# Kernel optimization log

Measured on AMD Instinct MI355X. Metric: run time of the kernel, lower is better.

Reference implementation:

```python
import jax, jax.numpy as jnp
import numpy as np

B, S, D = 1, 2048, 2048
H = 16            # num query heads
QL = 1536         # q_lora_rank
KVL = 512         # kv_lora_rank
DN = 128          # qk_nope_head_dim
DR = 64           # qk_rope_head_dim
DV = 128          # v_head_dim
F = 8192          # ffn intermediate
EPS = 1e-6
WAVE = 10000.0


def _rms(x, scale, eps=EPS):
    # fp32 norm then cast back, matching DeepSeekV3_1RMSNorm
    x32 = x.astype(jnp.float32)
    ms = jnp.mean(x32 * x32, axis=-1, keepdims=True)
    return (x32 * jax.lax.rsqrt(ms + eps)).astype(x.dtype) * scale


def _rope_tables(seq_len, dim):
    inv_freq = 1.0 / (WAVE ** (jnp.arange(0, dim, 2, dtype=jnp.float32) / dim))
    t = jnp.arange(seq_len, dtype=jnp.float32)[:, None] * inv_freq[None, :]  # [S, dim/2]
    emb = jnp.concatenate([t, t], axis=-1)  # [S, dim]
    return jnp.cos(emb), jnp.sin(emb)


def _apply_rope(x, cos, sin):
    # x: [B, S, H, dr]; rotate-half convention
    half = x.shape[-1] // 2
    x1, x2 = x[..., :half], x[..., half:]
    rot = jnp.concatenate([-x2, x1], axis=-1)
    return x * cos[None, :, None, :] + rot * sin[None, :, None, :]


def setup_inputs() -> dict:
    key = jax.random.key(0)
    ks = jax.random.split(key, 12)
    w = lambda k, shp: (jax.random.normal(k, shp, dtype=jnp.float32) * 0.02)
    inp = {
        "hidden_states": jax.random.normal(ks[0], (B, S, D), dtype=jnp.float32),
        "attention_mask": jnp.broadcast_to(jnp.tril(jnp.ones((S, S), dtype=bool)), (B, S, S)),
        "pre_attn_scale": jnp.ones((D,), jnp.float32),
        "wqa": w(ks[1], (D, QL)),
        "q_norm_scale": jnp.ones((QL,), jnp.float32),
        "wqb": w(ks[2], (QL, H * (DN + DR))),
        "wkva": w(ks[3], (D, KVL + DR)),
        "kv_norm_scale": jnp.ones((KVL,), jnp.float32),
        "wkvb": w(ks[4], (KVL, H * (DN + DV))),
        "wo": w(ks[5], (H * DV, D)),
        "pre_ffn_scale": jnp.ones((D,), jnp.float32),
        "wg": w(ks[6], (D, F)),
        "bg": jnp.zeros((F,), jnp.float32),
        "wu": w(ks[7], (D, F)),
        "bu": jnp.zeros((F,), jnp.float32),
        "wd": w(ks[8], (F, D)),
        "bd": jnp.zeros((D,), jnp.float32),
    }
    return inp


def reference(hidden_states, attention_mask, pre_attn_scale, wqa, q_norm_scale, wqb,
              wkva, kv_norm_scale, wkvb, wo, pre_ffn_scale, wg, bg, wu, bu, wd, bd):
    x = hidden_states
    # --- pre-attention RMSNorm ---
    n = _rms(x, pre_attn_scale)
    # --- MLA attention ---
    q = (_rms(n @ wqa, q_norm_scale) @ wqb).reshape(B, S, H, DN + DR)
    q_nope, q_rope = q[..., :DN], q[..., DN:]
    kva = n @ wkva                              # [B,S,KVL+DR]
    c_kv, k_rope = kva[..., :KVL], kva[..., KVL:]
    kv = (_rms(c_kv, kv_norm_scale) @ wkvb).reshape(B, S, H, DN + DV)
    k_nope, v = kv[..., :DN], kv[..., DN:]
    cos, sin = _rope_tables(S, DR)
    q_rope = _apply_rope(q_rope, cos, sin)
    k_rope = _apply_rope(k_rope[:, :, None, :], cos, sin)  # [B,S,1,DR] shared across heads
    qf = jnp.concatenate([q_nope, q_rope], axis=-1)
    kf = jnp.concatenate([k_nope, jnp.broadcast_to(k_rope, (B, S, H, DR))], axis=-1)
    scale = 1.0 / float(np.sqrt(DN + DR))
    scores = jnp.einsum('bqhd,bkhd->bhqk', qf, kf) * scale
    scores = jnp.where(attention_mask[:, None, :, :], scores, jnp.float32(-1e9))
    probs = jax.nn.softmax(scores, axis=-1)
    attn = jnp.einsum('bhqk,bkhd->bqhd', probs, v).reshape(B, S, H * DV)
    x = x + attn @ wo                            # residual 1 (dropout=0)
    # --- pre-FFN RMSNorm + dense SwiGLU FFN ---
    n = _rms(x, pre_ffn_scale)
    ff = (jax.nn.silu(n @ wg + bg) * (n @ wu + bu)) @ wd + bd
    return x + ff                                # residual 2
```

## Files before the change

kernel.cpp:

```cpp
#include <hip/hip_runtime.h>
#include <hip/hip_bf16.h>
#include <stdint.h>

typedef unsigned short u16;
using f32x4  = __attribute__((ext_vector_type(4))) float;
using bf16x8 = __attribute__((ext_vector_type(8))) __bf16;
using u32x4  = __attribute__((ext_vector_type(4))) uint32_t;
using u16x4  = __attribute__((ext_vector_type(4))) unsigned short;
using u16x8  = __attribute__((ext_vector_type(8))) unsigned short;

#define S_LEN 2048
#define DM    2048
#define NH    16
#define QLR   1536
#define KVLR  512
#define DNOPE 128
#define DROPE 64
#define DVAL  128
#define FFD   8192

static __device__ __forceinline__ float bf2f(u16 u) {
    union { uint32_t i; float f; } v; v.i = ((uint32_t)u) << 16; return v.f;
}
static __device__ __forceinline__ u16 f2bf(float f) {
    union { float f; uint32_t i; } v; v.f = f;
    uint32_t x = v.i;
    return (u16)((x + 0x7FFF + ((x >> 16) & 1)) >> 16);
}
static __device__ __forceinline__ void gload16(const u16* g, const u16* l) {
    __builtin_amdgcn_global_load_lds(
        (const __attribute__((address_space(1))) void*)g,
        (__attribute__((address_space(3))) void*)l, 16, 0, 0);
}

struct TWJob { const float* src; u16* dst; int R, C, xt, start; };
struct TWJobs { TWJob j[8]; };

__global__ __launch_bounds__(256)
void transpose_all(TWJobs jobs)
{
    __shared__ __align__(16) u16 tile[64][68];
    const int bid = blockIdx.x;
    int e = 0;
#pragma unroll
    for (int i = 1; i < 8; ++i) e = (bid >= jobs.j[i].start) ? i : e;
    const float* src = jobs.j[e].src;
    u16* dst = jobs.j[e].dst;
    const int R = jobs.j[e].R, C = jobs.j[e].C;
    const int local = bid - jobs.j[e].start;
    const int c0 = (local % jobs.j[e].xt) * 64;
    const int r0 = (local / jobs.j[e].xt) * 64;
    const int t = threadIdx.x;
#pragma unroll
    for (int i = 0; i < 4; ++i) {
        int idx = i * 256 + t;
        int r = idx >> 4, c4 = idx & 15;
        float4 v = *reinterpret_cast<const float4*>(&src[(size_t)(r0 + r) * C + c0 + c4 * 4]);
        u16x4 b; b[0] = f2bf(v.x); b[1] = f2bf(v.y); b[2] = f2bf(v.z); b[3] = f2bf(v.w);
        *reinterpret_cast<u16x4*>(&tile[r][c4 * 4]) = b;
    }
    __syncthreads();
#pragma unroll
    for (int i = 0; i < 4; ++i) {
        int idx = i * 256 + t;
        int rr = idx >> 4, k4 = idx & 15;
        u16x4 o;
#pragma unroll
        for (int j = 0; j < 4; ++j) o[j] = tile[k4 * 4 + j][rr];
        *reinterpret_cast<u16x4*>(&dst[(size_t)(c0 + rr) * R + r0 + k4 * 4]) = o;
    }
}

__global__ __launch_bounds__(256)
void transpose_v(const u16* __restrict__ kv, u16* __restrict__ vt)
{
    __shared__ __align__(16) u16 tile[64][76];
    const int t = threadIdx.x;
    const int s0 = blockIdx.x * 64;
    const int d0 = blockIdx.y * 64;
    const int h  = blockIdx.z;
#pragma unroll
    for (int i = 0; i < 2; ++i) {
        int idx = i * 256 + t;
        int s = idx >> 3, c8 = idx & 7;
        u16x8 v = *reinterpret_cast<const u16x8*>(kv + (size_t)(s0 + s) * (NH * 256) + h * 256 + 128 + d0 + c8 * 8);
        u16x4 lo, hi;
#pragma unroll
        for (int j = 0; j < 4; ++j) { lo[j] = v[j]; hi[j] = v[4 + j]; }
        *reinterpret_cast<u16x4*>(&tile[s][c8 * 8])     = lo;
        *reinterpret_cast<u16x4*>(&tile[s][c8 * 8 + 4]) = hi;
    }
    __syncthreads();
#pragma unroll
    for (int i = 0; i < 4; ++i) {
        int idx = i * 256 + t;
        int d = idx >> 4, s4 = idx & 15;
        u16x4 o;
#pragma unroll
        for (int j = 0; j < 4; ++j) o[j] = tile[s4 * 4 + j][d];
        *reinterpret_cast<u16x4*>(&vt[(size_t)(h * 128 + d0 + d) * S_LEN + s0 + s4 * 4]) = o;
    }
}

template<bool IN_F32>
__global__ __launch_bounds__(256)
void rms_norm(const void* __restrict__ in, int in_stride, int width,
              const float* __restrict__ scale, u16* __restrict__ out, int out_stride)
{
    const int row = blockIdx.x;
    const int t = threadIdx.x;
    const float* inf = (const float*)in;
    const u16*   inb = (const u16*)in;
    float ss = 0.f;
    for (int c = t; c < width; c += 256) {
        float v = IN_F32 ? inf[(size_t)row * in_stride + c] : bf2f(inb[(size_t)row * in_stride + c]);
        ss += v * v;
    }
#pragma unroll
    for (int o = 32; o > 0; o >>= 1) ss += __shfl_xor(ss, o);
    __shared__ float red[4];
    if ((t & 63) == 0) red[t >> 6] = ss;
    __syncthreads();
    float inv = rsqrtf((red[0] + red[1] + red[2] + red[3]) / (float)width + 1e-6f);
    for (int c = t; c < width; c += 256) {
        float v = IN_F32 ? inf[(size_t)row * in_stride + c] : bf2f(inb[(size_t)row * in_stride + c]);
        out[(size_t)row * out_stride + c] = f2bf(v * inv * scale[c]);
    }
}

__global__ __launch_bounds__(256)
void rope_qk(u16* __restrict__ q, const float* __restrict__ kva, u16* __restrict__ kr)
{
    const int s = blockIdx.x;
    const int t = threadIdx.x;
    for (int idx = t; idx < 544; idx += 256) {
        int d = idx & 31;
        float invf = powf(10000.f, -(float)(2 * d) / 64.f);
        float ang = (float)s * invf;
        float cs = cosf(ang), sn = sinf(ang);
        if (idx < 512) {
            int hh = idx >> 5;
            u16* base = q + ((size_t)s * NH + hh) * 192 + 128;
            float x1 = bf2f(base[d]), x2 = bf2f(base[d + 32]);
            base[d]      = f2bf(x1 * cs - x2 * sn);
            base[d + 32] = f2bf(x2 * cs + x1 * sn);
        } else {
            const float* kb = kva + (size_t)s * 576 + 512;
            float x1 = kb[d], x2 = kb[d + 32];
            kr[(size_t)s * 64 + d]      = f2bf(x1 * cs - x2 * sn);
            kr[(size_t)s * 64 + d + 32] = f2bf(x2 * cs + x1 * sn);
        }
    }
}

__global__ __launch_bounds__(256)
void init_out(const float* __restrict__ x2, const float* __restrict__ bd,
              float* __restrict__ out, int total4, int N)
{
    int i = blockIdx.x * 256 + threadIdx.x;
    const int stride = gridDim.x * 256;
    for (; i < total4; i += stride) {
        float4 r = ((const float4*)x2)[i];
        int col = (i * 4) & (N - 1);
        float4 b = *reinterpret_cast<const float4*>(&bd[col]);
        float4 o; o.x = r.x + b.x; o.y = r.y + b.y; o.z = r.z + b.z; o.w = r.w + b.w;
        ((float4*)out)[i] = o;
    }
}

template<int EPI>
__global__ __launch_bounds__(256)
void gemm_bt(const u16* __restrict__ A, const u16* __restrict__ BT,
             void* __restrict__ out, int M, int N, int K)
{
    __shared__ __align__(16) u16 As[128 * 64];
    __shared__ __align__(16) u16 Bs[128 * 64];
    const int t = threadIdx.x;
    const int lane = t & 63;
    const int w = t >> 6;
    const int wr = w >> 1, wc = w & 1;
    const int li = lane & 15;
    const int lg = lane >> 4;

    const int gx = gridDim.x;
    int nwg = gx * gridDim.y;
    int bid = blockIdx.y * gx + blockIdx.x;
    bid = (bid & 7) * (nwg >> 3) + (bid >> 3);
    const int m0 = (bid % gx) * 128;
    const int n0 = (bid / gx) * 128;

    const int nz = gridDim.z, z = blockIdx.z;
    const int nktt = K >> 6;
    const int qq = nktt / nz, rr = nktt % nz;
    const int kt0 = z * qq + (z < rr ? z : rr);
    const int ktEnd = kt0 + qq + (z < rr ? 1 : 0);

    const int srow = w * 32 + (lane >> 3);
    const int scol = (((lane & 7) ^ (lane >> 3)) << 3);
    const u16* ag = A  + (size_t)(m0 + srow) * K + scol;
    const u16* bg = BT + (size_t)(n0 + srow) * K + scol;

    f32x4 acc[4][4];
#pragma unroll
    for (int m = 0; m < 4; ++m)
#pragma unroll
        for (int n = 0; n < 4; ++n)
            acc[m][n] = f32x4{0.f, 0.f, 0.f, 0.f};

    for (int kt = kt0; kt < ktEnd; ++kt) {
        const int k0 = kt << 6;
        __syncthreads();
#pragma unroll
        for (int i = 0; i < 4; ++i) {
            gload16(ag + (size_t)i * 8 * K + k0, As + (w * 32 + i * 8) * 64);
            gload16(bg + (size_t)i * 8 * K + k0, Bs + (w * 32 + i * 8) * 64);
        }
        __syncthreads();
#pragma unroll
        for (int kk = 0; kk < 2; ++kk) {
            const int csw = (kk * 32 + lg * 8) ^ ((li & 7) << 3);
            bf16x8 af[4], bfr[4];
#pragma unroll
            for (int m = 0; m < 4; ++m)
                af[m] = *reinterpret_cast<const bf16x8*>(As + (wr * 64 + m * 16 + li) * 64 + csw);
#pragma unroll
            for (int n = 0; n < 4; ++n)
                bfr[n] = *reinterpret_cast<const bf16x8*>(Bs + (wc * 64 + n * 16 + li) * 64 + csw);
#pragma unroll
            for (int m = 0; m < 4; ++m)
#pragma unroll
                for (int n = 0; n < 4; ++n)
                    acc[m][n] = __builtin_amdgcn_mfma_f32_16x16x32_bf16(af[m], bfr[n], acc[m][n], 0, 0, 0);
        }
    }

#pragma unroll
    for (int m = 0; m < 4; ++m) {
        const int row = m0 + wr * 64 + m * 16 + lg * 4;
#pragma unroll
        for (int n = 0; n < 4; ++n) {
            const int col = n0 + wc * 64 + n * 16 + li;
            if (col < N) {
#pragma unroll
                for (int r2 = 0; r2 < 4; ++r2) {
                    float v = acc[m][n][r2];
                    size_t idx = (size_t)(row + r2) * N + col;
                    if (EPI == 0) ((u16*)out)[idx] = f2bf(v);
                    else          unsafeAtomicAdd((float*)out + idx, v);
                }
            }
        }
    }
}

template<int EPI>
__global__ __launch_bounds__(512, 4)
void gemm_big(const u16* __restrict__ A, const u16* __restrict__ BT,
              void* __restrict__ out, int M, int N, int K,
              const float* __restrict__ bias, const u16* __restrict__ gmul)
{
    __shared__ __align__(16) u16 As[256 * 64];
    __shared__ __align__(16) u16 Bs[128 * 64];
    const int t = threadIdx.x;
    const int lane = t & 63;
    const int w = t >> 6;
    const int wr = w >> 1, wc = w & 1;
    const int li = lane & 15;
    const int lg = lane >> 4;

    const int gx = gridDim.x;
    int nwg = gx * gridDim.y;
    int bid = blockIdx.y * gx + blockIdx.x;
    bid = (bid & 7) * (nwg >> 3) + (bid >> 3);
    const int m0 = (bid % gx) * 256;
    const int n0 = (bid / gx) * 128;

    const int nz = gridDim.z, z = blockIdx.z;
    const int nktt = K >> 6;
    const int qq = nktt / nz, rr = nktt % nz;
    const int kt0 = z * qq + (z < rr ? z : rr);
    const int ktEnd = kt0 + qq + (z < rr ? 1 : 0);

    const int sr = lane >> 3;
    const int scol = (((lane & 7) ^ sr) << 3);
    const u16* ag = A  + (size_t)(m0 + w * 8 + sr) * K + scol;
    const u16* bg = BT + (size_t)(n0 + w * 8 + sr) * K + scol;
    const u16* lA = As + (w * 8) * 64;
    const u16* lB = Bs + (w * 8) * 64;

    f32x4 acc[4][4];
#pragma unroll
    for (int m = 0; m < 4; ++m)
#pragma unroll
        for (int n = 0; n < 4; ++n)
            acc[m][n] = f32x4{0.f, 0.f, 0.f, 0.f};

    for (int kt = kt0; kt < ktEnd; ++kt) {
        const int k0 = kt << 6;
        __syncthreads();
#pragma unroll
        for (int i = 0; i < 4; ++i)
            gload16(ag + (size_t)i * 64 * K + k0, lA + i * 64 * 64);
#pragma unroll
        for (int i = 0; i < 2; ++i)
            gload16(bg + (size_t)i * 64 * K + k0, lB + i * 64 * 64);
        __syncthreads();
        __builtin_amdgcn_s_setprio(1);
#pragma unroll
        for (int kk = 0; kk < 2; ++kk) {
            const int csw = (kk * 32 + lg * 8) ^ ((li & 7) << 3);
            bf16x8 af[4], bfr[4];
#pragma unroll
            for (int m = 0; m < 4; ++m)
                af[m] = *reinterpret_cast<const bf16x8*>(As + (wr * 64 + m * 16 + li) * 64 + csw);
#pragma unroll
            for (int n = 0; n < 4; ++n)
                bfr[n] = *reinterpret_cast<const bf16x8*>(Bs + (wc * 64 + n * 16 + li) * 64 + csw);
#pragma unroll
            for (int m = 0; m < 4; ++m)
#pragma unroll
                for (int n = 0; n < 4; ++n)
                    acc[m][n] = __builtin_amdgcn_mfma_f32_16x16x32_bf16(af[m], bfr[n], acc[m][n], 0, 0, 0);
        }
        __builtin_amdgcn_s_setprio(0);
    }

#pragma unroll
    for (int m = 0; m < 4; ++m) {
        const int row = m0 + wr * 64 + m * 16 + lg * 4;
#pragma unroll
        for (int n = 0; n < 4; ++n) {
            const int col = n0 + wc * 64 + n * 16 + li;
#pragma unroll
            for (int r2 = 0; r2 < 4; ++r2) {
                float v = acc[m][n][r2];
                size_t idx = (size_t)(row + r2) * N + col;
                if (EPI == 0) {
                    ((u16*)out)[idx] = f2bf(v);
                } else if (EPI == 1) {
                    v += bias[col];
                    v = v / (1.f + __expf(-v));
                    ((u16*)out)[idx] = f2bf(v);
                } else if (EPI == 2) {
                    v = (v + bias[col]) * bf2f(gmul[idx]);
                    ((u16*)out)[idx] = f2bf(v);
                } else {
                    unsafeAtomicAdd((float*)out + idx, v);
                }
            }
        }
    }
}

__global__ __launch_bounds__(512)
void flash_attn(const u16* __restrict__ q, const u16* __restrict__ kv,
                const u16* __restrict__ kr, const u16* __restrict__ vt,
                u16* __restrict__ attn)
{
    __shared__ __align__(16) u16 KVs[2][20480];
    __shared__ __align__(16) u16 Ps[8][16][72];

    const int t = threadIdx.x;
    const int lane = t & 63;
    const int w = t >> 6;
    const int li = lane & 15;
    const int lg = lane >> 4;
    const int h = blockIdx.x;
    const int b = 15 - blockIdx.y;

    const int qt = (w < 4) ? (2 * b + 1) : (2 * b);
    const int my_nkt = qt + 1;
    const int block_nkt = 2 * b + 2;
    const int wl = w & 3;
    const int qr = qt * 64 + wl * 16;
    const int qpos = qr + li;

    auto stage = [&](int buf, int k0) {
        u16* base = &KVs[buf][0];
#pragma unroll
        for (int i = 0; i < 3; ++i) {
            int g = w * 3 + i;
            int P = g * 64 + lane;
            int j = P / 24, s = P % 24;
            int c = (s & 24) | ((s ^ (j & 7)) & 7);
            const u16* src = (c < 16)
                ? kv + (size_t)(k0 + j) * (NH * 256) + h * 256 + c * 8
                : kr + (size_t)(k0 + j) * 64 + (c - 16) * 8;
            gload16(src, base + g * 512);
        }
#pragma unroll
        for (int i = 0; i < 2; ++i) {
            int g = w * 2 + i;
            int P = g * 64 + lane;
            int d = P >> 3, s8 = P & 7;
            int c = s8 ^ (d & 7);
            const u16* src = vt + (size_t)(h * 128 + d) * S_LEN + k0 + c * 8;
            gload16(src, base + 12288 + g * 512);
        }
    };

    bf16x8 qf[6];
#pragma unroll
    for (int kb = 0; kb < 6; ++kb)
        qf[kb] = *reinterpret_cast<const bf16x8*>(q + ((size_t)(qr + li) * NH + h) * 192 + kb * 32 + lg * 8);

    f32x4 oacc[8];
#pragma unroll
    for (int i = 0; i < 8; ++i) oacc[i] = f32x4{0.f, 0.f, 0.f, 0.f};
    float m_run = -INFINITY, l_run = 0.f;

    stage(0, 0);
    int buf = 0;
    const float scale = 0.07216878364870322f;

    for (int kt = 0; kt < block_nkt; ++kt) {
        const int k0 = kt << 6;
        __syncthreads();
        if (kt + 1 < block_nkt) stage(buf ^ 1, (kt + 1) << 6);

        if (kt < my_nkt) {
            const u16* bb = &KVs[buf][0];

            f32x4 sacc[4];
#pragma unroll
            for (int jt = 0; jt < 4; ++jt) sacc[jt] = f32x4{0.f, 0.f, 0.f, 0.f};
            __builtin_amdgcn_s_setprio(1);
#pragma unroll
            for (int kb = 0; kb < 6; ++kb) {
                const int c = kb * 4 + lg;
                const int s = (c & 24) | ((c ^ (li & 7)) & 7);
#pragma unroll
                for (int jt = 0; jt < 4; ++jt) {
                    bf16x8 kf = *reinterpret_cast<const bf16x8*>(bb + ((jt * 16 + li) * 24 + s) * 8);
                    sacc[jt] = __builtin_amdgcn_mfma_f32_16x16x32_bf16(kf, qf[kb], sacc[jt], 0, 0, 0);
                }
            }
            __builtin_amdgcn_s_setprio(0);

            float p[16];
            float mt = -INFINITY;
            if (k0 + 63 <= qr) {
#pragma unroll
                for (int jt = 0; jt < 4; ++jt)
#pragma unroll
                    for (int r = 0; r < 4; ++r) {
                        float sv = sacc[jt][r] * scale;
                        p[jt * 4 + r] = sv;
                        mt = fmaxf(mt, sv);
                    }
            } else {
#pragma unroll
                for (int jt = 0; jt < 4; ++jt)
#pragma unroll
                    for (int r = 0; r < 4; ++r) {
                        int jpos = k0 + jt * 16 + lg * 4 + r;
                        float sv = (jpos <= qpos) ? sacc[jt][r] * scale : -INFINITY;
                        p[jt * 4 + r] = sv;
                        mt = fmaxf(mt, sv);
                    }
            }
            mt = fmaxf(mt, __shfl_xor(mt, 16));
            mt = fmaxf(mt, __shfl_xor(mt, 32));
            if (!__all(mt <= m_run + 8.f)) {
                float mn = fmaxf(m_run, mt);
                float sf = __expf(m_run - mn);
                float sfr[4];
#pragma unroll
                for (int r = 0; r < 4; ++r)
                    sfr[r] = __shfl(sf, (lane & 48) + lg * 4 + r);
#pragma unroll
                for (int d2 = 0; d2 < 8; ++d2)
#pragma unroll
                    for (int r = 0; r < 4; ++r)
                        oacc[d2][r] *= sfr[r];
                l_run *= sf;
                m_run = mn;
            }
            float rsum = 0.f;
#pragma unroll
            for (int i2 = 0; i2 < 16; ++i2) { p[i2] = __expf(p[i2] - m_run); rsum += p[i2]; }
            rsum += __shfl_xor(rsum, 16);
            rsum += __shfl_xor(rsum, 32);
            l_run += rsum;

#pragma unroll
            for (int jt = 0; jt < 4; ++jt) {
                u16x4 pk;
                pk[0] = f2bf(p[jt * 4 + 0]); pk[1] = f2bf(p[jt * 4 + 1]);
                pk[2] = f2bf(p[jt * 4 + 2]); pk[3] = f2bf(p[jt * 4 + 3]);
                *reinterpret_cast<u16x4*>(&Ps[w][li][jt * 16 + lg * 4]) = pk;
            }

            __builtin_amdgcn_s_setprio(1);
#pragma unroll
            for (int ks = 0; ks < 2; ++ks) {
                bf16x8 pf = *reinterpret_cast<const bf16x8*>(&Ps[w][li][ks * 32 + lg * 8]);
                const int vs = (ks * 4 + lg) ^ (li & 7);
#pragma unroll
                for (int d2 = 0; d2 < 8; ++d2) {
                    bf16x8 vf = *reinterpret_cast<const bf16x8*>(bb + 12288 + ((d2 * 16 + li) * 8 + vs) * 8);
                    oacc[d2] = __builtin_amdgcn_mfma_f32_16x16x32_bf16(pf, vf, oacc[d2], 0, 0, 0);
                }
            }
            __builtin_amdgcn_s_setprio(0);
        }
        buf ^= 1;
    }

    float rl = 1.f / l_run;
    float rlr[4];
#pragma unroll
    for (int r = 0; r < 4; ++r)
        rlr[r] = __shfl(rl, (lane & 48) + lg * 4 + r);
#pragma unroll
    for (int d2 = 0; d2 < 8; ++d2)
#pragma unroll
        for (int r = 0; r < 4; ++r) {
            int srow = qr + lg * 4 + r;
            int dcol = d2 * 16 + li;
            attn[(size_t)srow * (NH * DVAL) + h * DVAL + dcol] = f2bf(oacc[d2][r] * rlr[r]);
        }
}

extern "C" void kernel_launch(void* const* d_in, const int* in_sizes, int n_in,
                              void* d_out, int out_size, void* d_ws, size_t ws_size,
                              hipStream_t stream)
{
    const float* hidden   = (const float*)d_in[0];
    const float* pa_scale = (const float*)d_in[2];
    const float* wqa      = (const float*)d_in[3];
    const float* qn_scale = (const float*)d_in[4];
    const float* wqb      = (const float*)d_in[5];
    const float* wkva     = (const float*)d_in[6];
    const float* kv_scale = (const float*)d_in[7];
    const float* wkvb     = (const float*)d_in[8];
    const float* wo       = (const float*)d_in[9];
    const float* pf_scale = (const float*)d_in[10];
    const float* wg       = (const float*)d_in[11];
    const float* bg       = (const float*)d_in[12];
    const float* wu       = (const float*)d_in[13];
    const float* bu       = (const float*)d_in[14];
    const float* wd       = (const float*)d_in[15];
    const float* bd       = (const float*)d_in[16];
    float* out = (float*)d_out;

    size_t off = 0;
    auto alloc = [&](size_t bytes) {
        off = (off + 255) & ~(size_t)255;
        void* p = (char*)d_ws + off;
        off += bytes;
        return p;
    };
    u16* wqaT  = (u16*)alloc((size_t)QLR * DM * 2);
    u16* wqbT  = (u16*)alloc((size_t)3072 * QLR * 2);
    u16* wkvaT = (u16*)alloc((size_t)640 * DM * 2);
    u16* wkvbT = (u16*)alloc((size_t)4096 * KVLR * 2);
    u16* woT   = (u16*)alloc((size_t)DM * DM * 2);
    u16* wgT   = (u16*)alloc((size_t)FFD * DM * 2);
    u16* wuT   = (u16*)alloc((size_t)FFD * DM * 2);
    u16* wdT   = (u16*)alloc((size_t)DM * FFD * 2);
    u16* n1    = (u16*)alloc((size_t)S_LEN * DM * 2);
    float* qlora32 = (float*)alloc((size_t)S_LEN * QLR * 4);
    float* kva32   = (float*)alloc((size_t)S_LEN * 576 * 4);
    u16* qn    = (u16*)alloc((size_t)S_LEN * QLR * 2);
    u16* qbuf  = (u16*)alloc((size_t)S_LEN * 3072 * 2);
    u16* ckvn  = (u16*)alloc((size_t)S_LEN * KVLR * 2);
    u16* kvbuf = (u16*)alloc((size_t)S_LEN * 4096 * 2);
    u16* krbuf = (u16*)alloc((size_t)S_LEN * 64 * 2);
    u16* attnb = (u16*)alloc((size_t)S_LEN * DM * 2);
    float* x2  = (float*)alloc((size_t)S_LEN * DM * 4);
    u16* n2    = (u16*)alloc((size_t)S_LEN * DM * 2);
    u16* gbuf  = (u16*)alloc((size_t)S_LEN * FFD * 2);
    u16* hbuf  = (u16*)alloc((size_t)S_LEN * FFD * 2);
    u16* vtb = (u16*)qlora32;
    (void)ws_size; (void)in_sizes; (void)n_in; (void)out_size;

    TWJobs jobs;
    int startAcc = 0;
    auto setJob = [&](int i, const float* s, u16* d, int R, int C) {
        jobs.j[i] = TWJob{s, d, R, C, C / 64, startAcc};
        startAcc += (C / 64) * (R / 64);
    };
    setJob(0, wqa,  wqaT,  2048, 1536);
    setJob(1, wqb,  wqbT,  1536, 3072);
    setJob(2, wkva, wkvaT, 2048,  576);
    setJob(3, wkvb, wkvbT,  512, 4096);
    setJob(4, wo,   woT,   2048, 2048);
    setJob(5, wg,   wgT,   2048, 8192);
    setJob(6, wu,   wuT,   2048, 8192);
    setJob(7, wd,   wdT,   8192, 2048);
    hipLaunchKernelGGL(transpose_all, dim3(startAcc), 256, 0, stream, jobs);

    hipMemsetAsync(qlora32, 0, (size_t)S_LEN * QLR * 4, stream);
    hipMemsetAsync(kva32,   0, (size_t)S_LEN * 576 * 4, stream);

    hipLaunchKernelGGL((rms_norm<true>),  dim3(S_LEN), 256, 0, stream, hidden, DM, DM, pa_scale, n1, DM);

    hipLaunchKernelGGL((gemm_bt<5>), dim3(16, 12, 2), 256, 0, stream, n1, wqaT, qlora32, S_LEN, QLR, DM);
    hipLaunchKernelGGL((gemm_bt<5>), dim3(16,  5, 4), 256, 0, stream, n1, wkvaT, kva32, S_LEN, 576, DM);
    hipLaunchKernelGGL((rms_norm<true>), dim3(S_LEN), 256, 0, stream, qlora32, QLR, QLR, qn_scale, qn, QLR);
    hipLaunchKernelGGL((gemm_bt<0>), dim3(16, 24), 256, 0, stream, qn, wqbT, qbuf, S_LEN, 3072, QLR);
    hipLaunchKernelGGL((rms_norm<true>), dim3(S_LEN), 256, 0, stream, kva32, 576, KVLR, kv_scale, ckvn, KVLR);
    hipLaunchKernelGGL(rope_qk, dim3(S_LEN), 256, 0, stream, qbuf, kva32, krbuf);
    hipLaunchKernelGGL((gemm_big<0>), dim3(8, 32), 512, 0, stream, ckvn, wkvbT, kvbuf, S_LEN, 4096, KVLR, nullptr, nullptr);

    hipLaunchKernelGGL(transpose_v, dim3(S_LEN/64, 2, NH), 256, 0, stream, kvbuf, vtb);
    hipLaunchKernelGGL(flash_attn, dim3(NH, 16), 512, 0, stream, qbuf, kvbuf, krbuf, vtb, attnb);

    hipMemcpyAsync(x2, hidden, (size_t)S_LEN * DM * 4, hipMemcpyDeviceToDevice, stream);
    hipLaunchKernelGGL((gemm_big<5>), dim3(8, 16, 4), 512, 0, stream, attnb, woT, x2, S_LEN, DM, DM, nullptr, nullptr);

    hipLaunchKernelGGL((rms_norm<true>), dim3(S_LEN), 256, 0, stream, x2, DM, DM, pf_scale, n2, DM);

    hipLaunchKernelGGL(init_out, dim3(2048), 256, 0, stream, x2, bd, out, S_LEN * DM / 4, DM);
    hipLaunchKernelGGL((gemm_big<1>), dim3(8, 64), 512, 0, stream, n2, wgT, gbuf, S_LEN, FFD, DM, bg, nullptr);
    hipLaunchKernelGGL((gemm_big<2>), dim3(8, 64), 512, 0, stream, n2, wuT, hbuf, S_LEN, FFD, DM, bu, gbuf);
    hipLaunchKernelGGL((gemm_big<5>), dim3(8, 16, 4), 512, 0, stream, hbuf, wdT, out, S_LEN, DM, FFD, nullptr, nullptr);
}
```

Baseline: 644.8 us.

## Run gate and up GEMMs in one launch, multiply separately, raise split-K

Replaces the two sequential gate/up FFN GEMMs (the second reading the first's output in its epilogue) with one gemm_gu launch. The z grid axis selects gate or up weights, so both run concurrently, and a separate elementwise kernel multiplies them into the hidden buffer. It also raises the split-K factor for the q/kv down-projections and for the wo/wd atomic-add GEMMs to spread more work across CUs. The trade-off is an extra full pass over two 2048x8192 bf16 buffers plus more atomic traffic. The new GEMM is a simpler single-buffered kernel, and the up output aliases a scratch buffer much smaller than it needs.

```diff
diff --git a/kernel.cpp b/kernel.cpp
--- a/kernel.cpp
+++ b/kernel.cpp
@@ -168,6 +168,22 @@
     }
 }
 
+__global__ __launch_bounds__(256)
+void mul_gu(const u16* __restrict__ g, const u16* __restrict__ u,
+            u16* __restrict__ h, int total8)
+{
+    int i = blockIdx.x * 256 + threadIdx.x;
+    const int stride = gridDim.x * 256;
+    for (; i < total8; i += stride) {
+        u16x8 gv = ((const u16x8*)g)[i];
+        u16x8 uv = ((const u16x8*)u)[i];
+        u16x8 hv;
+#pragma unroll
+        for (int j = 0; j < 8; ++j) hv[j] = f2bf(bf2f(gv[j]) * bf2f(uv[j]));
+        ((u16x8*)h)[i] = hv;
+    }
+}
+
 template<int EPI>
 __global__ __launch_bounds__(256)
 void gemm_bt(const u16* __restrict__ A, const u16* __restrict__ BT,
@@ -341,12 +357,97 @@
                     v += bias[col];
                     v = v / (1.f + __expf(-v));
                     ((u16*)out)[idx] = f2bf(v);
-                } else if (EPI == 2) {
-                    v = (v + bias[col]) * bf2f(gmul[idx]);
-                    ((u16*)out)[idx] = f2bf(v);
                 } else {
                     unsafeAtomicAdd((float*)out + idx, v);
                 }
+            }
+        }
+    }
+}
+
+__global__ __launch_bounds__(512, 4)
+void gemm_gu(const u16* __restrict__ A, const u16* __restrict__ BgT, const u16* __restrict__ BuT,
+             u16* __restrict__ gout, u16* __restrict__ uout, int M, int N, int K,
+             const float* __restrict__ bg, const float* __restrict__ bu)
+{
+    __shared__ __align__(16) u16 As[256 * 64];
+    __shared__ __align__(16) u16 Bs[128 * 64];
+    const int t = threadIdx.x;
+    const int lane = t & 63;
+    const int w = t >> 6;
+    const int wr = w >> 1, wc = w & 1;
+    const int li = lane & 15;
+    const int lg = lane >> 4;
+    const int isUp = blockIdx.z;
+
+    const u16* BT = isUp ? BuT : BgT;
+    const float* bias = isUp ? bu : bg;
+    u16* out = isUp ? uout : gout;
+
+    const int gx = gridDim.x;
+    int nwg = gx * gridDim.y;
+    int bid = blockIdx.y * gx + blockIdx.x;
+    bid = (bid & 7) * (nwg >> 3) + (bid >> 3);
+    const int m0 = (bid % gx) * 256;
+    const int n0 = (bid / gx) * 128;
+
+    const int sr = lane >> 3;
+    const int scol = (((lane & 7) ^ sr) << 3);
+    const u16* ag = A  + (size_t)(m0 + w * 8 + sr) * K + scol;
+    const u16* bgp = BT + (size_t)(n0 + w * 8 + sr) * K + scol;
+    const u16* lA = As + (w * 8) * 64;
+    const u16* lB = Bs + (w * 8) * 64;
+
+    f32x4 acc[4][4];
+#pragma unroll
+    for (int m = 0; m < 4; ++m)
+#pragma unroll
+        for (int n = 0; n < 4; ++n)
+            acc[m][n] = f32x4{0.f, 0.f, 0.f, 0.f};
+
+    const int nkt = K >> 6;
+    for (int kt = 0; kt < nkt; ++kt) {
+        const int k0 = kt << 6;
+        __syncthreads();
+#pragma unroll
+        for (int i = 0; i < 4; ++i)
+            gload16(ag + (size_t)i * 64 * K + k0, lA + i * 64 * 64);
+#pragma unroll
+        for (int i = 0; i < 2; ++i)
+            gload16(bgp + (size_t)i * 64 * K + k0, lB + i * 64 * 64);
+        __syncthreads();
+        __builtin_amdgcn_s_setprio(1);
+#pragma unroll
+        for (int kk = 0; kk < 2; ++kk) {
+            const int csw = (kk * 32 + lg * 8) ^ ((li & 7) << 3);
+            bf16x8 af[4], bfr[4];
+#pragma unroll
+            for (int m = 0; m < 4; ++m)
+                af[m] = *reinterpret_cast<const bf16x8*>(As + (wr * 64 + m * 16 + li) * 64 + csw);
+#pragma unroll
+            for (int n = 0; n < 4; ++n)
+                bfr[n] = *reinterpret_cast<const bf16x8*>(Bs + (wc * 64 + n * 16 + li) * 64 + csw);
+#pragma unroll
+            for (int m = 0; m < 4; ++m)
+#pragma unroll
+                for (int n = 0; n < 4; ++n)
+                    acc[m][n] = __builtin_amdgcn_mfma_f32_16x16x32_bf16(af[m], bfr[n], acc[m][n], 0, 0, 0);
+        }
+        __builtin_amdgcn_s_setprio(0);
+    }
+
+#pragma unroll
+    for (int m = 0; m < 4; ++m) {
+        const int row = m0 + wr * 64 + m * 16 + lg * 4;
+#pragma unroll
+        for (int n = 0; n < 4; ++n) {
+            const int col = n0 + wc * 64 + n * 16 + li;
+            float bv = bias[col];
+#pragma unroll
+            for (int r2 = 0; r2 < 4; ++r2) {
+                float v = acc[m][n][r2] + bv;
+                if (!isUp) v = v / (1.f + __expf(-v));
+                ((u16*)out)[(size_t)(row + r2) * N + col] = f2bf(v);
             }
         }
     }
@@ -572,7 +673,8 @@
     u16* n2    = (u16*)alloc((size_t)S_LEN * DM * 2);
     u16* gbuf  = (u16*)alloc((size_t)S_LEN * FFD * 2);
     u16* hbuf  = (u16*)alloc((size_t)S_LEN * FFD * 2);
-    u16* vtb = (u16*)qlora32;
+    u16* vtb  = (u16*)qlora32;
+    u16* ubuf = (u16*)qlora32;
     (void)ws_size; (void)in_sizes; (void)n_in; (void)out_size;
 
     TWJobs jobs;
@@ -596,8 +698,8 @@
 
     hipLaunchKernelGGL((rms_norm<true>),  dim3(S_LEN), 256, 0, stream, hidden, DM, DM, pa_scale, n1, DM);
 
-    hipLaunchKernelGGL((gemm_bt<5>), dim3(16, 12, 2), 256, 0, stream, n1, wqaT, qlora32, S_LEN, QLR, DM);
-    hipLaunchKernelGGL((gemm_bt<5>), dim3(16,  5, 4), 256, 0, stream, n1, wkvaT, kva32, S_LEN, 576, DM);
+    hipLaunchKernelGGL((gemm_bt<5>), dim3(16, 12, 4), 256, 0, stream, n1, wqaT, qlora32, S_LEN, QLR, DM);
+    hipLaunchKernelGGL((gemm_bt<5>), dim3(16,  5, 8), 256, 0, stream, n1, wkvaT, kva32, S_LEN, 576, DM);
     hipLaunchKernelGGL((rms_norm<true>), dim3(S_LEN), 256, 0, stream, qlora32, QLR, QLR, qn_scale, qn, QLR);
     hipLaunchKernelGGL((gemm_bt<0>), dim3(16, 24), 256, 0, stream, qn, wqbT, qbuf, S_LEN, 3072, QLR);
     hipLaunchKernelGGL((rms_norm<true>), dim3(S_LEN), 256, 0, stream, kva32, 576, KVLR, kv_scale, ckvn, KVLR);
@@ -608,12 +710,12 @@
     hipLaunchKernelGGL(flash_attn, dim3(NH, 16), 512, 0, stream, qbuf, kvbuf, krbuf, vtb, attnb);
 
     hipMemcpyAsync(x2, hidden, (size_t)S_LEN * DM * 4, hipMemcpyDeviceToDevice, stream);
-    hipLaunchKernelGGL((gemm_big<5>), dim3(8, 16, 4), 512, 0, stream, attnb, woT, x2, S_LEN, DM, DM, nullptr, nullptr);
+    hipLaunchKernelGGL((gemm_big<5>), dim3(8, 16, 6), 512, 0, stream, attnb, woT, x2, S_LEN, DM, DM, nullptr, nullptr);
 
     hipLaunchKernelGGL((rms_norm<true>), dim3(S_LEN), 256, 0, stream, x2, DM, DM, pf_scale, n2, DM);
 
     hipLaunchKernelGGL(init_out, dim3(2048), 256, 0, stream, x2, bd, out, S_LEN * DM / 4, DM);
-    hipLaunchKernelGGL((gemm_big<1>), dim3(8, 64), 512, 0, stream, n2, wgT, gbuf, S_LEN, FFD, DM, bg, nullptr);
-    hipLaunchKernelGGL((gemm_big<2>), dim3(8, 64), 512, 0, stream, n2, wuT, hbuf, S_LEN, FFD, DM, bu, gbuf);
-    hipLaunchKernelGGL((gemm_big<5>), dim3(8, 16, 4), 512, 0, stream, hbuf, wdT, out, S_LEN, DM, FFD, nullptr, nullptr);
-}
+    hipLaunchKernelGGL(gemm_gu, dim3(8, 64, 2), 512, 0, stream, n2, wgT, wuT, gbuf, ubuf, S_LEN, FFD, DM, bg, bu);
+    hipLaunchKernelGGL(mul_gu, dim3(2048), 256, 0, stream, gbuf, ubuf, hbuf, S_LEN * FFD / 8);
+    hipLaunchKernelGGL((gemm_big<5>), dim3(8, 16, 6), 512, 0, stream, hbuf, wdT, out, S_LEN, DM, FFD, nullptr, nullptr);
+}
```

Result: slower. 733.2 us (+13.7%).
